# Kernel optimization log

Hardware: AMD Instinct MI355X
Metric: run time of the kernel (lower is better)

The kernel has to match this reference:

```python
import jax, jax.numpy as jnp
import numpy as np

B, T, D, TY = 64, 512, 96, 512
H, DK = 4, 32            # num_heads, embed_dim_per_head
E = H * DK               # embed_dim = 128
P = 2                    # function='L' -> 2 coefficients
L, HID = 64, 128         # latent_dim, hidden_dim


def setup_inputs() -> dict:
    key = jax.random.key(0)
    ks = jax.random.split(key, 16)
    inp = {
        "timesteps": jax.random.uniform(ks[0], (B, T), jnp.float32),
        "X": jax.random.normal(ks[1], (B, T, D), jnp.float32),
        "M": jax.random.randint(ks[2], (B, T, D), 0, 2).astype(jnp.float32),
        "y_time_steps": jax.random.uniform(ks[3], (B, TY), jnp.float32),
        # time_embedding: Linear(1, E)
        "te_w": jax.random.normal(ks[4], (E,), jnp.float32),
        "te_b": jax.random.normal(ks[5], (E,), jnp.float32) * 0.1,
        # learned query [1, P, E]
        "query": jax.random.normal(ks[6], (1, P, E), jnp.float32),
        # query_map / key_map: Linear(E, E), stored [in, out]
        "q_w": jax.random.normal(ks[7], (E, E), jnp.float32) / np.sqrt(E),
        "q_b": jax.random.normal(ks[8], (E,), jnp.float32) * 0.1,
        "k_w": jax.random.normal(ks[9], (E, E), jnp.float32) / np.sqrt(E),
        "k_b": jax.random.normal(ks[10], (E,), jnp.float32) * 0.1,
        # attn shared out: Linear(2D*H, L)
        "ow": jax.random.normal(ks[11], (2 * D * H, L), jnp.float32) / np.sqrt(2 * D * H),
        "ob": jnp.zeros((L,), jnp.float32),
        # decoder MLP: Linear(L,HID)+ReLU+Linear(HID,D)
        "w1": jax.random.normal(ks[12], (L, HID), jnp.float32) / np.sqrt(L),
        "b1": jnp.zeros((HID,), jnp.float32),
        "w2": jax.random.normal(ks[13], (HID, D), jnp.float32) / np.sqrt(HID),
        "b2": jnp.zeros((D,), jnp.float32),
    }
    return inp


def _fld_forward(timesteps, X, M, y_time_steps, te_w, te_b, query,
                 q_w, q_b, k_w, k_b, ow, ob, w1, b1, w2, b2):
    b, t, d = X.shape
    # time embedding: Linear(1,E), sin applied to indices i % H == 0
    emb = timesteps[..., None] * te_w + te_b               # [B,T,E]
    sin_idx = (jnp.arange(E) % H) == 0
    emb = jnp.where(sin_idx, jnp.sin(emb), emb)

    X_cat = jnp.concatenate([X, M], axis=-1)               # [B,T,2D]
    M_cat = jnp.concatenate([M, M], axis=-1)               # [B,T,2D]

    q = query @ q_w + q_b                                   # [1,P,E]
    k = emb @ k_w + k_b                                     # [B,T,E]
    q = q.reshape(1, P, H, DK).transpose(0, 2, 1, 3)        # [1,H,P,dk]
    k = k.reshape(b, t, H, DK).transpose(0, 2, 1, 3)        # [B,H,T,dk]

    scores = jnp.einsum('xhpd,bhtd->bhpt', q, k) / np.sqrt(DK)  # [B,H,P,T]
    # broadcast over value feature dim, mask per-feature, softmax over T
    logits = jnp.where(M_cat[:, None, None, :, :] == 0, -jnp.inf,
                       scores[..., None])                   # [B,H,P,T,2D]
    p = jax.nn.softmax(logits, axis=-2)
    xa = jnp.einsum('bhptf,btf->bhpf', p, X_cat)            # [B,H,P,2D]
    xa = xa.transpose(0, 2, 1, 3).reshape(b, P, H * 2 * d)  # [B,P,H*2D]
    coeffs = xa @ ow + ob                                   # [B,P,L]

    # function 'L': linear in y_time_steps
    x = coeffs[:, 0][:, None, :] + y_time_steps[:, :, None] * coeffs[:, 1][:, None, :]
    h1 = jax.nn.relu(x @ w1 + b1)
    return h1 @ w2 + b2                                     # [B,TY,D]


def reference(timesteps, X, M, y_time_steps, te_w, te_b, query,
              q_w, q_b, k_w, k_b, ow, ob, w1, b1, w2, b2):
    return _fld_forward(timesteps, X, M, y_time_steps, te_w, te_b, query,
                        q_w, q_b, k_w, k_b, ow, ob, w1, b1, w2, b2)
```

## Files before the change

### kernel.cpp

```cpp
#include <hip/hip_runtime.h>
#include <math.h>

#define B_   64
#define T_   512
#define D_   96
#define TY_  512
#define H_   4
#define DK_  32
#define E_   128
#define P_   2
#define L_   64
#define HID_ 128

#define WS_OB2P  1024
#define WS_PN    2048
#define WS_PD    395264
#define WS_TAB   1048576
#define RSZ_     25088
#define TABOFF   256

__global__ __launch_bounds__(256) void kphase1(
    const float* __restrict__ tsteps, const float* __restrict__ te_w,
    const float* __restrict__ te_b,   const float* __restrict__ X,
    const float* __restrict__ M,      const float* __restrict__ query,
    const float* __restrict__ q_w,    const float* __restrict__ q_b,
    const float* __restrict__ k_w,    const float* __restrict__ k_b,
    const float* __restrict__ ow,     float* __restrict__ ws)
{
    const int bi = blockIdx.x, tid = threadIdx.x;
    const int c = bi & 7, b = bi >> 3;

    __shared__ float qm[P_ * E_];
    __shared__ float w2q_s[E_ * 8];
    __shared__ float tw_s[E_], tb_s[E_], bq_s[8];
    __shared__ float w_sB[64][8];
    __shared__ float red[96 * 17];
    __shared__ float obp2[4][64];

    {
        int p = tid >> 7, ep = tid & 127;
        float acc = q_b[ep];
        #pragma unroll 4
        for (int e = 0; e < E_; ++e)
            acc += query[p * E_ + e] * q_w[e * E_ + ep];
        qm[p * E_ + ep] = acc;
    }
    if (tid < E_) { tw_s[tid] = te_w[tid]; tb_s[tid] = te_b[tid]; }
    __syncthreads();
    const float rs = 0.17677669529663687f;
    #pragma unroll
    for (int i = 0; i < 4; ++i) {
        int idx = tid + i * 256;
        int e = idx >> 3, hp = idx & 7, h = hp >> 1, p = hp & 1;
        float acc = 0.f;
        #pragma unroll
        for (int dk = 0; dk < DK_; ++dk)
            acc += k_w[e * E_ + h * DK_ + dk] * qm[p * E_ + h * DK_ + dk];
        w2q_s[idx] = acc * rs;
    }
    if (tid < 8) {
        int hp = tid, h = hp >> 1, p = hp & 1;
        float acc = 0.f;
        #pragma unroll
        for (int dk = 0; dk < DK_; ++dk)
            acc += k_b[h * DK_ + dk] * qm[p * E_ + h * DK_ + dk];
        bq_s[hp] = acc * rs;
    }
    __syncthreads();

    {
        const int t = tid & 63, hpg = tid >> 6, hp0 = hpg * 2;
        const float tv = tsteps[b * T_ + c * 64 + t];
        float a0 = 0.f, a1 = 0.f;
        #pragma unroll 4
        for (int e = 0; e < E_; ++e) {
            float v = tv * tw_s[e] + tb_s[e];
            if ((e & 3) == 0) v = __sinf(v);
            float2 w = *(const float2*)&w2q_s[e * 8 + hp0];
            a0 += v * w.x;
            a1 += v * w.y;
        }
        float e0 = __expf(a0 + bq_s[hp0]);
        float e1 = __expf(a1 + bq_s[hp0 + 1]);
        *(float2*)&w_sB[t][hp0] = make_float2(e0, e1);
    }
    __syncthreads();

    const int fid = tid & 127, slice = tid >> 7;
    float num[8] = {0.f, 0.f, 0.f, 0.f, 0.f, 0.f, 0.f, 0.f};
    float den[8] = {0.f, 0.f, 0.f, 0.f, 0.f, 0.f, 0.f, 0.f};
    if (fid < 96) {
        #pragma unroll 4
        for (int i = 0; i < 32; ++i) {
            int tl = slice + 2 * i;
            size_t base = ((size_t)(b * T_ + c * 64 + tl)) * D_ + fid;
            float m = M[base], x = X[base];
            float mx = m * x;
            float4 wa = *(const float4*)&w_sB[tl][0];
            float4 wb = *(const float4*)&w_sB[tl][4];
            float wv[8];
            *(float4*)&wv[0] = wa; *(float4*)&wv[4] = wb;
            #pragma unroll
            for (int hp = 0; hp < 8; ++hp) {
                num[hp] += wv[hp] * mx;
                den[hp] += wv[hp] * m;
            }
        }
    }
    __syncthreads();
    if (slice == 1 && fid < 96) {
        #pragma unroll
        for (int hp = 0; hp < 8; ++hp) {
            red[fid * 17 + hp]     = num[hp];
            red[fid * 17 + 8 + hp] = den[hp];
        }
    }
    __syncthreads();
    if (slice == 0 && fid < 96) {
        float* pN = ws + WS_PN + ((size_t)((b * 8 + c) * 8)) * 96;
        float* pD = ws + WS_PD + ((size_t)((b * 8 + c) * 8)) * 96;
        #pragma unroll
        for (int hp = 0; hp < 8; ++hp) {
            pN[hp * 96 + fid] = num[hp] + red[fid * 17 + hp];
            pD[hp * 96 + fid] = den[hp] + red[fid * 17 + 8 + hp];
        }
    }

    if (b == 0) {
        int sub = tid >> 6, l = tid & 63;
        float acc = 0.f;
        #pragma unroll
        for (int k = 0; k < 12; ++k) {
            int hj = c * 48 + sub * 12 + k;
            int h = hj / 96, j = hj - h * 96;
            acc += ow[(size_t)(h * 2 * D_ + D_ + j) * L_ + l];
        }
        obp2[sub][l] = acc;
        __syncthreads();
        if (sub == 0)
            ws[WS_OB2P + c * 64 + l] = obp2[0][l] + obp2[1][l]
                                     + obp2[2][l] + obp2[3][l];
    }
}

__global__ __launch_bounds__(256) void kab(
    const float* __restrict__ ow, const float* __restrict__ ob,
    const float* __restrict__ w1, const float* __restrict__ b1,
    const float* __restrict__ w2, const float* __restrict__ b2,
    float* __restrict__ ws)
{
    __shared__ float w2_s[HID_ * D_];
    __shared__ float xa_s[8 * 96];
    __shared__ float cfp[4][2][64];
    __shared__ float cf_s[2][64];
    __shared__ float abp[2][2][128];
    __shared__ float ab0_s[HID_], ab1_s[HID_];
    __shared__ float t_s[HID_], u_s[HID_], vt_s[HID_], c0_s[HID_];
    __shared__ int   sidx_s[HID_];
    __shared__ float base0_s[96], base1_s[96];

    const int b = blockIdx.x, tid = threadIdx.x;

    {
        const float4* src = (const float4*)w2;
        float4* dst = (float4*)w2_s;
        #pragma unroll
        for (int i = 0; i < 12; ++i) dst[tid + i * 256] = src[tid + i * 256];
    }

    #pragma unroll
    for (int it = 0; it < 3; ++it) {
        int flat = tid + it * 256;
        int hp = flat / 96, f = flat - hp * 96;
        float n = 0.f, d = 0.f;
        #pragma unroll
        for (int cc = 0; cc < 8; ++cc) {
            n += ws[WS_PN + ((size_t)((b * 8 + cc) * 8 + hp)) * 96 + f];
            d += ws[WS_PD + ((size_t)((b * 8 + cc) * 8 + hp)) * 96 + f];
        }
        xa_s[flat] = n / d;
    }
    __syncthreads();

    #pragma unroll
    for (int it = 0; it < 2; ++it) {
        int idx = tid + it * 256;
        int h = idx >> 7, p = (idx >> 6) & 1, l = idx & 63;
        const float* xr = xa_s + (h * 2 + p) * 96;
        const float* owr = ow + (size_t)(h * 2 * D_) * L_ + l;
        float acc = 0.f;
        #pragma unroll 4
        for (int f = 0; f < 96; ++f)
            acc += xr[f] * owr[(size_t)f * L_];
        cfp[h][p][l] = acc;
    }
    __syncthreads();

    if (tid < 128) {
        int p = tid >> 6, l = tid & 63;
        float v = cfp[0][p][l] + cfp[1][p][l] + cfp[2][p][l]
                + cfp[3][p][l] + ob[l];
        #pragma unroll
        for (int g = 0; g < 8; ++g) v += ws[WS_OB2P + g * 64 + l];
        cf_s[p][l] = v;
    }
    __syncthreads();

    {
        int s = tid >> 7, j = tid & 127;
        float a0 = 0.f, a1 = 0.f;
        #pragma unroll 4
        for (int li = 0; li < 32; ++li) {
            int l = s * 32 + li;
            float wv = w1[l * HID_ + j];
            a0 += cf_s[0][l] * wv;
            a1 += cf_s[1][l] * wv;
        }
        abp[s][0][j] = a0;
        abp[s][1][j] = a1;
    }
    __syncthreads();

    if (tid < 128) {
        ab0_s[tid] = abp[0][0][tid] + abp[1][0][tid] + b1[tid];
    } else {
        int j = tid - 128;
        ab1_s[j] = abp[0][1][j] + abp[1][1][j];
    }
    __syncthreads();

    if (tid < 128) {
        float a0 = ab0_s[tid], a1 = ab1_s[tid];
        float t, u, vt, c0;
        if (a1 > 0.f)      { t = -a0 / a1;  u =  a1; vt = -a0; c0 = 0.f; }
        else if (a1 < 0.f) { t = -a0 / a1;  u = -a1; vt =  a0; c0 = 0.f; }
        else               { t = INFINITY;  u = 0.f; vt = 0.f; c0 = fabsf(a0); }
        t_s[tid] = t; u_s[tid] = u; vt_s[tid] = vt; c0_s[tid] = c0;
    }
    __syncthreads();

    if (tid < 128) {
        float tj = t_s[tid];
        int r = 0;
        for (int k = 0; k < 128; ++k) {
            float tk = t_s[k];
            r += (tk < tj) || (tk == tj && k < tid);
        }
        sidx_s[r] = tid;
    }
    __syncthreads();

    float* reg = ws + WS_TAB + (size_t)b * RSZ_;
    if (tid < 96) {
        float g0 = 0.f, g1 = 0.f, ut = 0.f, vta = 0.f, cc2 = 0.f;
        #pragma unroll 4
        for (int j = 0; j < 128; ++j) {
            float wv = w2_s[j * 96 + tid];
            g0  += ab0_s[j] * wv;
            g1  += ab1_s[j] * wv;
            ut  += u_s[j]  * wv;
            vta += vt_s[j] * wv;
            cc2 += c0_s[j] * wv;
        }
        base0_s[tid] = 0.5f * (g0 + cc2 + vta) + b2[tid];
        base1_s[tid] = 0.5f * (g1 - ut);
    } else if (tid >= 128) {
        int k = tid - 128;
        reg[k] = t_s[sidx_s[k]];
    }
    __syncthreads();

    if (tid < 96) {
        float cur0 = base0_s[tid], cur1 = base1_s[tid];
        float* tb = reg + TABOFF;
        tb[tid] = cur0;
        tb[96 + tid] = cur1;
        #pragma unroll 4
        for (int k = 0; k < 128; ++k) {
            int j = sidx_s[k];
            float wv = w2_s[j * 96 + tid];
            cur0 -= vt_s[j] * wv;
            cur1 += u_s[j] * wv;
            tb[(k + 1) * 192 + tid]      = cur0;
            tb[(k + 1) * 192 + 96 + tid] = cur1;
        }
    }
}

__global__ __launch_bounds__(256) void kdec(
    const float* __restrict__ yts, const float* __restrict__ ws,
    float* __restrict__ out)
{
    __shared__ float tS[128];
    const int bi = blockIdx.x, tid = threadIdx.x;
    const int b = bi >> 4;
    const float* reg = ws + WS_TAB + (size_t)b * RSZ_;
    if (tid < 128) tS[tid] = reg[tid];
    __syncthreads();

    const int pos = tid >> 3, d0 = (tid & 7) * 12;
    const float y = yts[bi * 32 + pos];

    int lo = 0, hi = 128;
    #pragma unroll
    for (int s = 0; s < 7; ++s) {
        int mid = (lo + hi) >> 1;
        if (tS[mid] < y) lo = mid + 1; else hi = mid;
    }

    const float* R = reg + TABOFF + lo * 192 + d0;
    float* op = out + ((size_t)(bi * 32 + pos)) * D_ + d0;
    #pragma unroll
    for (int q = 0; q < 3; ++q) {
        float4 r0 = *(const float4*)(R + q * 4);
        float4 r1 = *(const float4*)(R + 96 + q * 4);
        float4 v;
        v.x = r0.x + y * r1.x;
        v.y = r0.y + y * r1.y;
        v.z = r0.z + y * r1.z;
        v.w = r0.w + y * r1.w;
        *(float4*)(op + q * 4) = v;
    }
}

extern "C" void kernel_launch(void* const* d_in, const int* in_sizes, int n_in,
                              void* d_out, int out_size, void* d_ws, size_t ws_size,
                              hipStream_t stream)
{
    const float* timesteps = (const float*)d_in[0];
    const float* X         = (const float*)d_in[1];
    const float* M         = (const float*)d_in[2];
    const float* yts       = (const float*)d_in[3];
    const float* te_w      = (const float*)d_in[4];
    const float* te_b      = (const float*)d_in[5];
    const float* query     = (const float*)d_in[6];
    const float* q_w       = (const float*)d_in[7];
    const float* q_b       = (const float*)d_in[8];
    const float* k_w       = (const float*)d_in[9];
    const float* k_b       = (const float*)d_in[10];
    const float* ow        = (const float*)d_in[11];
    const float* ob        = (const float*)d_in[12];
    const float* w1        = (const float*)d_in[13];
    const float* b1        = (const float*)d_in[14];
    const float* w2        = (const float*)d_in[15];
    const float* b2        = (const float*)d_in[16];
    float* out = (float*)d_out;
    float* ws  = (float*)d_ws;

    kphase1<<<512, 256, 0, stream>>>(timesteps, te_w, te_b, X, M, query,
                                     q_w, q_b, k_w, k_b, ow, ws);
    kab<<<B_, 256, 0, stream>>>(ow, ob, w1, b1, w2, b2, ws);
    kdec<<<(B_ * TY_) / 32, 256, 0, stream>>>(yts, ws, out);
}
```

Measured before the change: 165.6 us.

## Fuse coefficient and decode kernels into a sorted-query sweep per batch

Replaces the separate coefficient kernel and the table-lookup decoder with one 512-thread kernel per batch. It rank-sorts the 512 y time steps in shared memory, then sweeps them in order, applying each ReLU breakpoint incrementally and writing outputs directly. This removes the per-batch piecewise-linear table written to and read back from global memory, plus one kernel launch. In exchange, all output writes come from only 64 blocks running a serial loop, and each batch pays an O(n²) rank sort. Two small unroll-factor tweaks are also included.

```diff
diff --git a/kernel.cpp b/kernel.cpp
--- a/kernel.cpp
+++ b/kernel.cpp
@@ -15,9 +15,6 @@
 #define WS_OB2P  1024
 #define WS_PN    2048
 #define WS_PD    395264
-#define WS_TAB   1048576
-#define RSZ_     25088
-#define TABOFF   256
 
 __global__ __launch_bounds__(256) void kphase1(
     const float* __restrict__ tsteps, const float* __restrict__ te_w,
@@ -40,7 +37,7 @@
     {
         int p = tid >> 7, ep = tid & 127;
         float acc = q_b[ep];
-        #pragma unroll 4
+        #pragma unroll 8
         for (int e = 0; e < E_; ++e)
             acc += query[p * E_ + e] * q_w[e * E_ + ep];
         qm[p * E_ + ep] = acc;
@@ -143,17 +140,21 @@
     }
 }
 
-__global__ __launch_bounds__(256) void kab(
+__global__ __launch_bounds__(512) void ksweep(
     const float* __restrict__ ow, const float* __restrict__ ob,
     const float* __restrict__ w1, const float* __restrict__ b1,
-    const float* __restrict__ w2, const float* __restrict__ b2,
-    float* __restrict__ ws)
+    const float* __restrict__ yts, const float* __restrict__ w2,
+    const float* __restrict__ b2, const float* __restrict__ ws,
+    float* __restrict__ out)
 {
     __shared__ float w2_s[HID_ * D_];
-    __shared__ float xa_s[8 * 96];
-    __shared__ float cfp[4][2][64];
+    union Scr {
+        struct { float xa[768]; float cfp[4][2][64]; float abp[2][2][128]; } e;
+        struct { float ysv[512]; int ysi[512]; float ts[128]; } l;
+    };
+    __shared__ Scr scr;
+    __shared__ float yload_s[512];
     __shared__ float cf_s[2][64];
-    __shared__ float abp[2][2][128];
     __shared__ float ab0_s[HID_], ab1_s[HID_];
     __shared__ float t_s[HID_], u_s[HID_], vt_s[HID_], c0_s[HID_];
     __shared__ int   sidx_s[HID_];
@@ -165,12 +166,11 @@
         const float4* src = (const float4*)w2;
         float4* dst = (float4*)w2_s;
         #pragma unroll
-        for (int i = 0; i < 12; ++i) dst[tid + i * 256] = src[tid + i * 256];
-    }
-
-    #pragma unroll
-    for (int it = 0; it < 3; ++it) {
-        int flat = tid + it * 256;
+        for (int i = 0; i < 6; ++i) dst[tid + i * 512] = src[tid + i * 512];
+    }
+    yload_s[tid] = yts[b * TY_ + tid];
+
+    for (int flat = tid; flat < 8 * 96; flat += 512) {
         int hp = flat / 96, f = flat - hp * 96;
         float n = 0.f, d = 0.f;
         #pragma unroll
@@ -178,35 +178,33 @@
             n += ws[WS_PN + ((size_t)((b * 8 + cc) * 8 + hp)) * 96 + f];
             d += ws[WS_PD + ((size_t)((b * 8 + cc) * 8 + hp)) * 96 + f];
         }
-        xa_s[flat] = n / d;
-    }
-    __syncthreads();
-
-    #pragma unroll
-    for (int it = 0; it < 2; ++it) {
-        int idx = tid + it * 256;
-        int h = idx >> 7, p = (idx >> 6) & 1, l = idx & 63;
-        const float* xr = xa_s + (h * 2 + p) * 96;
+        scr.e.xa[flat] = n / d;
+    }
+    __syncthreads();
+
+    {
+        int h = tid >> 7, p = (tid >> 6) & 1, l = tid & 63;
+        const float* xr = scr.e.xa + (h * 2 + p) * 96;
         const float* owr = ow + (size_t)(h * 2 * D_) * L_ + l;
         float acc = 0.f;
-        #pragma unroll 4
+        #pragma unroll 8
         for (int f = 0; f < 96; ++f)
             acc += xr[f] * owr[(size_t)f * L_];
-        cfp[h][p][l] = acc;
+        scr.e.cfp[h][p][l] = acc;
     }
     __syncthreads();
 
     if (tid < 128) {
         int p = tid >> 6, l = tid & 63;
-        float v = cfp[0][p][l] + cfp[1][p][l] + cfp[2][p][l]
-                + cfp[3][p][l] + ob[l];
+        float v = scr.e.cfp[0][p][l] + scr.e.cfp[1][p][l] + scr.e.cfp[2][p][l]
+                + scr.e.cfp[3][p][l] + ob[l];
         #pragma unroll
         for (int g = 0; g < 8; ++g) v += ws[WS_OB2P + g * 64 + l];
         cf_s[p][l] = v;
     }
     __syncthreads();
 
-    {
+    if (tid < 256) {
         int s = tid >> 7, j = tid & 127;
         float a0 = 0.f, a1 = 0.f;
         #pragma unroll 4
@@ -216,16 +214,16 @@
             a0 += cf_s[0][l] * wv;
             a1 += cf_s[1][l] * wv;
         }
-        abp[s][0][j] = a0;
-        abp[s][1][j] = a1;
+        scr.e.abp[s][0][j] = a0;
+        scr.e.abp[s][1][j] = a1;
     }
     __syncthreads();
 
     if (tid < 128) {
-        ab0_s[tid] = abp[0][0][tid] + abp[1][0][tid] + b1[tid];
-    } else {
+        ab0_s[tid] = scr.e.abp[0][0][tid] + scr.e.abp[1][0][tid] + b1[tid];
+    } else if (tid < 256) {
         int j = tid - 128;
-        ab1_s[j] = abp[0][1][j] + abp[1][1][j];
+        ab1_s[j] = scr.e.abp[0][1][j] + scr.e.abp[1][1][j];
     }
     __syncthreads();
 
@@ -237,11 +235,23 @@
         else               { t = INFINITY;  u = 0.f; vt = 0.f; c0 = fabsf(a0); }
         t_s[tid] = t; u_s[tid] = u; vt_s[tid] = vt; c0_s[tid] = c0;
     }
+    {
+        float y = yload_s[tid];
+        int r = 0;
+        #pragma unroll 8
+        for (int k = 0; k < 512; ++k) {
+            float yk = yload_s[k];
+            r += (yk < y) || (yk == y && k < tid);
+        }
+        scr.l.ysv[r] = y;
+        scr.l.ysi[r] = tid;
+    }
     __syncthreads();
 
     if (tid < 128) {
         float tj = t_s[tid];
         int r = 0;
+        #pragma unroll 8
         for (int k = 0; k < 128; ++k) {
             float tk = t_s[k];
             r += (tk < tj) || (tk == tj && k < tid);
@@ -250,7 +260,6 @@
     }
     __syncthreads();
 
-    float* reg = ws + WS_TAB + (size_t)b * RSZ_;
     if (tid < 96) {
         float g0 = 0.f, g1 = 0.f, ut = 0.f, vta = 0.f, cc2 = 0.f;
         #pragma unroll 4
@@ -264,62 +273,32 @@
         }
         base0_s[tid] = 0.5f * (g0 + cc2 + vta) + b2[tid];
         base1_s[tid] = 0.5f * (g1 - ut);
-    } else if (tid >= 128) {
+    } else if (tid >= 128 && tid < 256) {
         int k = tid - 128;
-        reg[k] = t_s[sidx_s[k]];
-    }
-    __syncthreads();
-
-    if (tid < 96) {
-        float cur0 = base0_s[tid], cur1 = base1_s[tid];
-        float* tb = reg + TABOFF;
-        tb[tid] = cur0;
-        tb[96 + tid] = cur1;
-        #pragma unroll 4
-        for (int k = 0; k < 128; ++k) {
-            int j = sidx_s[k];
-            float wv = w2_s[j * 96 + tid];
-            cur0 -= vt_s[j] * wv;
-            cur1 += u_s[j] * wv;
-            tb[(k + 1) * 192 + tid]      = cur0;
-            tb[(k + 1) * 192 + 96 + tid] = cur1;
-        }
-    }
-}
-
-__global__ __launch_bounds__(256) void kdec(
-    const float* __restrict__ yts, const float* __restrict__ ws,
-    float* __restrict__ out)
-{
-    __shared__ float tS[128];
-    const int bi = blockIdx.x, tid = threadIdx.x;
-    const int b = bi >> 4;
-    const float* reg = ws + WS_TAB + (size_t)b * RSZ_;
-    if (tid < 128) tS[tid] = reg[tid];
-    __syncthreads();
-
-    const int pos = tid >> 3, d0 = (tid & 7) * 12;
-    const float y = yts[bi * 32 + pos];
-
-    int lo = 0, hi = 128;
-    #pragma unroll
-    for (int s = 0; s < 7; ++s) {
-        int mid = (lo + hi) >> 1;
-        if (tS[mid] < y) lo = mid + 1; else hi = mid;
-    }
-
-    const float* R = reg + TABOFF + lo * 192 + d0;
-    float* op = out + ((size_t)(bi * 32 + pos)) * D_ + d0;
-    #pragma unroll
-    for (int q = 0; q < 3; ++q) {
-        float4 r0 = *(const float4*)(R + q * 4);
-        float4 r1 = *(const float4*)(R + 96 + q * 4);
-        float4 v;
-        v.x = r0.x + y * r1.x;
-        v.y = r0.y + y * r1.y;
-        v.z = r0.z + y * r1.z;
-        v.w = r0.w + y * r1.w;
-        *(float4*)(op + q * 4) = v;
+        scr.l.ts[k] = t_s[sidx_s[k]];
+    }
+    __syncthreads();
+
+    {
+        const int seg = tid >> 7, dd = tid & 127;
+        if (dd < 96) {
+            float cur0 = base0_s[dd], cur1 = base1_s[dd];
+            int ptr = 0;
+            const int i0 = seg * 128, i1 = i0 + 128;
+            #pragma unroll 1
+            for (int i = i0; i < i1; ++i) {
+                float y = scr.l.ysv[i];
+                while (ptr < 128 && scr.l.ts[ptr] < y) {
+                    int j = sidx_s[ptr];
+                    float wv = w2_s[j * 96 + dd];
+                    cur0 -= vt_s[j] * wv;
+                    cur1 += u_s[j] * wv;
+                    ++ptr;
+                }
+                int pos = scr.l.ysi[i];
+                out[((size_t)(b * TY_ + pos)) * D_ + dd] = cur0 + y * cur1;
+            }
+        }
     }
 }
 
@@ -349,6 +328,5 @@
 
     kphase1<<<512, 256, 0, stream>>>(timesteps, te_w, te_b, X, M, query,
                                      q_w, q_b, k_w, k_b, ow, ws);
-    kab<<<B_, 256, 0, stream>>>(ow, ob, w1, b1, w2, b2, ws);
-    kdec<<<(B_ * TY_) / 32, 256, 0, stream>>>(yts, ws, out);
+    ksweep<<<B_, 512, 0, stream>>>(ow, ob, w1, b1, yts, w2, b2, ws, out);
 }
```

Measured after the change: 185.9 us. +12.3%, slower.
